# Kernel tuning notes

Hardware: AMD Instinct MI355X
Metric: run time of the kernel (lower is better)

## Reference

```python
import jax, jax.numpy as jnp
import numpy as np

D_MODEL = 2048
NUM_HEADS = 16
HEAD_DIM = D_MODEL // NUM_HEADS


def setup_inputs() -> dict:
    key = jax.random.key(0)
    ks = jax.random.split(key, 11)
    B, S = 2, 2048
    scale = 1.0 / np.sqrt(D_MODEL)
    inp = {
        "q": jax.random.normal(ks[0], (B, S, D_MODEL), jnp.float32),
        "k": jax.random.normal(ks[1], (B, S, D_MODEL), jnp.float32),
        "v": jax.random.normal(ks[2], (B, S, D_MODEL), jnp.float32),
        "Wq": jax.random.normal(ks[3], (D_MODEL, D_MODEL), jnp.float32) * scale,
        "bq": jnp.zeros((D_MODEL,), jnp.float32),
        "Wk": jax.random.normal(ks[4], (D_MODEL, D_MODEL), jnp.float32) * scale,
        "bk": jnp.zeros((D_MODEL,), jnp.float32),
        "Wv": jax.random.normal(ks[5], (D_MODEL, D_MODEL), jnp.float32) * scale,
        "bv": jnp.zeros((D_MODEL,), jnp.float32),
        "Wo": jax.random.normal(ks[6], (D_MODEL, D_MODEL), jnp.float32) * scale,
        "bo": jnp.zeros((D_MODEL,), jnp.float32),
    }
    return inp


def reference(q, k, v, Wq, bq, Wk, bk, Wv, bv, Wo, bo):
    B, S, _ = q.shape
    # projections (torch Linear: x @ W.T + b)
    qh = (q @ Wq.T + bq).reshape(B, S, NUM_HEADS, HEAD_DIM).transpose(0, 2, 1, 3)
    kh = (k @ Wk.T + bk).reshape(B, S, NUM_HEADS, HEAD_DIM).transpose(0, 2, 1, 3)
    vh = (v @ Wv.T + bv).reshape(B, S, NUM_HEADS, HEAD_DIM).transpose(0, 2, 1, 3)
    # scaled dot-product attention, full O(S^2) scores as in original
    scores = jnp.einsum("bhqd,bhkd->bhqk", qh, kh) / jnp.sqrt(
        jnp.asarray(HEAD_DIM, jnp.float32)
    )
    attn = jax.nn.softmax(scores, axis=-1)
    out = jnp.einsum("bhqk,bhkd->bhqd", attn, vh)
    out = out.transpose(0, 2, 1, 3).reshape(B, S, D_MODEL)
    return out @ Wo.T + bo
```

## Files before the change

### kernel.cpp

```cpp
#include <hip/hip_runtime.h>


typedef __attribute__((ext_vector_type(8))) short bf16x8;
typedef __attribute__((ext_vector_type(4))) float f32x4;
typedef __attribute__((ext_vector_type(8))) unsigned short u16x8;

__device__ __forceinline__ unsigned short f2bf(float f) {
  unsigned int u = __float_as_uint(f);
  u += 0x7fffu + ((u >> 16) & 1u);
  return (unsigned short)(u >> 16);
}

#if __has_builtin(__builtin_amdgcn_cvt_pk_bf16_f32)
__device__ __forceinline__ unsigned int pack2bf(float x, float y) {
  auto r = __builtin_amdgcn_cvt_pk_bf16_f32(x, y);
  return __builtin_bit_cast(unsigned int, r);
}
#else
__device__ __forceinline__ unsigned int pack2bf(float x, float y) {
  return (unsigned int)f2bf(x) | ((unsigned int)f2bf(y) << 16);
}
#endif

__device__ __forceinline__ float fast_exp2(float x) {
#if __has_builtin(__builtin_amdgcn_exp2f)
  return __builtin_amdgcn_exp2f(x);
#else
  return exp2f(x);
#endif
}

__device__ __forceinline__ void async16(const void* g, void* l) {
  __builtin_amdgcn_global_load_lds(
      (const __attribute__((address_space(1))) unsigned int*)g,
      (__attribute__((address_space(3))) unsigned int*)l, 16, 0, 0);
}

__device__ __forceinline__ f32x4 mfma_bf16(bf16x8 a, bf16x8 b, f32x4 c) {
  return __builtin_amdgcn_mfma_f32_16x16x32_bf16(a, b, c, 0, 0, 0);
}

__global__ __launch_bounds__(256) void cvt_kernel(
    const float* __restrict__ q, const float* __restrict__ k,
    const float* __restrict__ v, const float* __restrict__ Wq,
    const float* __restrict__ Wk, const float* __restrict__ Wv,
    const float* __restrict__ Wo, unsigned short* __restrict__ Xq,
    unsigned short* __restrict__ Xk, unsigned short* __restrict__ Xv,
    unsigned short* __restrict__ WqB, unsigned short* __restrict__ WkB,
    unsigned short* __restrict__ WvB, unsigned short* __restrict__ WoB) {
  size_t i = ((size_t)blockIdx.x * 256 + threadIdx.x) * 8;
  const float* src;
  unsigned short* dst;
  size_t off;
  if (i < 8388608ull) { src = q; dst = Xq; off = i; }
  else if (i < 16777216ull) { src = k; dst = Xk; off = i - 8388608ull; }
  else if (i < 25165824ull) { src = v; dst = Xv; off = i - 16777216ull; }
  else if (i < 29360128ull) { src = Wq; dst = WqB; off = i - 25165824ull; }
  else if (i < 33554432ull) { src = Wk; dst = WkB; off = i - 29360128ull; }
  else if (i < 37748736ull) { src = Wv; dst = WvB; off = i - 33554432ull; }
  else { src = Wo; dst = WoB; off = i - 37748736ull; }
  f32x4 a = *(const f32x4*)(src + off);
  f32x4 b = *(const f32x4*)(src + off + 4);
  u16x8 r;
  r[0] = f2bf(a[0]); r[1] = f2bf(a[1]); r[2] = f2bf(a[2]); r[3] = f2bf(a[3]);
  r[4] = f2bf(b[0]); r[5] = f2bf(b[1]); r[6] = f2bf(b[2]); r[7] = f2bf(b[3]);
  *(u16x8*)(dst + off) = r;
}

__device__ __forceinline__ void gemm_core_k2048(
    const unsigned short* __restrict__ A, const unsigned short* __restrict__ Bm,
    int m0, int n0, unsigned short* As, unsigned short* Bs,
    f32x4 (&acc)[4][4]) {
  const int tid = threadIdx.x;
  const int lane = tid & 63;
  const int wave = tid >> 6;
  const int quad = lane >> 4;
  const int l15 = lane & 15;
  const int wmt = (wave >> 1) * 4;
  const int wnt = (wave & 1) * 4;
  const int K = 2048;

  auto stage = [&](int kt, int buf) {
    unsigned short* SA = As + buf * (128 * 64);
    unsigned short* SB = Bs + buf * (128 * 64);
#pragma unroll
    for (int p = 0; p < 4; ++p) {
      int x = p * 256 + tid;
      int row = ((x >> 7) << 4) + ((x >> 3) & 15);
      int gk = kt + (((x & 7) ^ ((x >> 3) & 7)) << 3);
      async16(A + (size_t)(m0 + row) * K + gk,
              (char*)SA + (size_t)(p * 256 + wave * 64) * 16);
      async16(Bm + (size_t)(n0 + row) * K + gk,
              (char*)SB + (size_t)(p * 256 + wave * 64) * 16);
    }
  };
  stage(0, 0);
#pragma unroll 1
  for (int it = 0; it < 32; ++it) {
    __syncthreads();
    if (it + 1 < 32) stage((it + 1) * 64, (it + 1) & 1);
    const unsigned short* SA = As + (it & 1) * (128 * 64);
    const unsigned short* SB = Bs + (it & 1) * (128 * 64);
#pragma unroll
    for (int s = 0; s < 2; ++s) {
      const int cs = (s * 4 + quad) ^ (l15 & 7);
      bf16x8 af[4], bfr[4];
#pragma unroll
      for (int t = 0; t < 4; ++t) {
        af[t] = *(const bf16x8*)(SA + ((wmt + t) * 128 + l15 * 8 + cs) * 8);
        bfr[t] = *(const bf16x8*)(SB + ((wnt + t) * 128 + l15 * 8 + cs) * 8);
      }
#pragma unroll
      for (int mt = 0; mt < 4; ++mt)
#pragma unroll
        for (int nt = 0; nt < 4; ++nt)
          acc[mt][nt] = mfma_bf16(af[mt], bfr[nt], acc[mt][nt]);
    }
  }
}

__global__ __launch_bounds__(256, 2) void qkv_gemm(
    const unsigned short* __restrict__ Xq, const unsigned short* __restrict__ Xk,
    const unsigned short* __restrict__ Xv, const unsigned short* __restrict__ Wq,
    const unsigned short* __restrict__ Wk, const unsigned short* __restrict__ Wv,
    const float* __restrict__ bq, const float* __restrict__ bk,
    const float* __restrict__ bv, unsigned short* __restrict__ Qb,
    unsigned short* __restrict__ Kb, unsigned short* __restrict__ Vt) {
  __shared__ unsigned short As[2][128 * 64];
  __shared__ unsigned short Bs[2][128 * 64];
  const int z = blockIdx.z;
  const unsigned short* A = z == 0 ? Xq : z == 1 ? Xk : Xv;
  const unsigned short* Bm = z == 0 ? Wq : z == 1 ? Wk : Wv;
  const float* bias = z == 0 ? bq : z == 1 ? bk : bv;
  const int m0 = blockIdx.y * 128;
  const int n0 = blockIdx.x * 128;

  f32x4 acc[4][4];
#pragma unroll
  for (int i = 0; i < 4; ++i)
#pragma unroll
    for (int j = 0; j < 4; ++j) acc[i][j] = f32x4{0.f, 0.f, 0.f, 0.f};
  gemm_core_k2048(A, Bm, m0, n0, As[0], Bs[0], acc);

  const int lane = threadIdx.x & 63;
  const int wave = threadIdx.x >> 6;
  const int quad = lane >> 4;
  const int l15 = lane & 15;
  const int wmt = (wave >> 1) * 4;
  const int wnt = (wave & 1) * 4;
  const float SK = z == 0 ? 0.12753102331285527f : 1.0f;
  const int N = 2048;

#pragma unroll
  for (int nt = 0; nt < 4; ++nt) {
    int col = n0 + (wnt + nt) * 16 + l15;
    float bv_ = bias[col];
    if (z == 2) {
      int h = col >> 7, d = col & 127;
#pragma unroll
      for (int mt = 0; mt < 4; ++mt) {
        int row0 = m0 + (wmt + mt) * 16 + quad * 4;
        int bb = row0 >> 11, s = row0 & 2047;
        uint2 pk;
        pk.x = pack2bf(acc[mt][nt][0] + bv_, acc[mt][nt][1] + bv_);
        pk.y = pack2bf(acc[mt][nt][2] + bv_, acc[mt][nt][3] + bv_);
        *(uint2*)(Vt + ((size_t)((bb * 16 + h) * 128 + d)) * 2048 + s) = pk;
      }
    } else {
      unsigned short* C = z == 0 ? Qb : Kb;
#pragma unroll
      for (int mt = 0; mt < 4; ++mt) {
        int row0 = m0 + (wmt + mt) * 16 + quad * 4;
#pragma unroll
        for (int r = 0; r < 4; ++r)
          C[(size_t)(row0 + r) * N + col] = f2bf((acc[mt][nt][r] + bv_) * SK);
      }
    }
  }
}

__global__ __launch_bounds__(256, 2) void o_gemm(
    const unsigned short* __restrict__ A, const unsigned short* __restrict__ Bm,
    const float* __restrict__ bias, float* __restrict__ Cf) {
  __shared__ unsigned short As[2][128 * 64];
  __shared__ unsigned short Bs[2][128 * 64];
  const int m0 = blockIdx.y * 128;
  const int n0 = blockIdx.x * 128;

  f32x4 acc[4][4];
#pragma unroll
  for (int i = 0; i < 4; ++i)
#pragma unroll
    for (int j = 0; j < 4; ++j) acc[i][j] = f32x4{0.f, 0.f, 0.f, 0.f};
  gemm_core_k2048(A, Bm, m0, n0, As[0], Bs[0], acc);

  const int lane = threadIdx.x & 63;
  const int wave = threadIdx.x >> 6;
  const int quad = lane >> 4;
  const int l15 = lane & 15;
  const int wmt = (wave >> 1) * 4;
  const int wnt = (wave & 1) * 4;
  const int N = 2048;
#pragma unroll
  for (int nt = 0; nt < 4; ++nt) {
    int col = n0 + (wnt + nt) * 16 + l15;
    float bv_ = bias[col];
#pragma unroll
    for (int mt = 0; mt < 4; ++mt) {
      int row0 = m0 + (wmt + mt) * 16 + quad * 4;
#pragma unroll
      for (int r = 0; r < 4; ++r)
        Cf[(size_t)(row0 + r) * N + col] = acc[mt][nt][r] + bv_;
    }
  }
}

__global__ __launch_bounds__(256, 2) void attn_kernel(
    const unsigned short* __restrict__ Qg, const unsigned short* __restrict__ Kg,
    const unsigned short* __restrict__ Vt, unsigned short* __restrict__ ctx) {
  __shared__ unsigned short Ks[2][64 * 128];
  __shared__ unsigned short Vs[2][128 * 64];
  __shared__ unsigned short Ps[128 * 64];
  const int tid = threadIdx.x;
  const int lane = tid & 63;
  const int wave = tid >> 6;
  const int quad = lane >> 4;
  const int l15 = lane & 15;
  const int qt = blockIdx.x, h = blockIdx.y, b = blockIdx.z;
  const int q0 = qt * 128;
  const int swz = (l15 & 7) * 8;

  bf16x8 aq[2][4];
#pragma unroll
  for (int mt = 0; mt < 2; ++mt) {
    const unsigned short* qrow =
        Qg + (size_t)(b * 2048 + q0 + wave * 32 + mt * 16 + l15) * 2048 + h * 128;
#pragma unroll
    for (int ks = 0; ks < 4; ++ks)
      aq[mt][ks] = *(const bf16x8*)(qrow + ks * 32 + quad * 8);
  }

  f32x4 o[2][8];
#pragma unroll
  for (int mt = 0; mt < 2; ++mt)
#pragma unroll
    for (int dt = 0; dt < 8; ++dt) o[mt][dt] = f32x4{0.f, 0.f, 0.f, 0.f};
  f32x4 lacc[2] = {f32x4{0.f, 0.f, 0.f, 0.f}, f32x4{0.f, 0.f, 0.f, 0.f}};

  auto stage = [&](int t, int buf) {
#pragma unroll
    for (int p = 0; p < 4; ++p) {
      int slot = p * 256 + tid;
      {
        int nt = slot >> 8, c = (slot >> 4) & 15, r15 = slot & 15;
        const unsigned short* g =
            Kg + (size_t)(b * 2048 + t * 64 + nt * 16 + r15) * 2048 + h * 128 + c * 8;
        async16(g, (char*)Ks[buf] + (size_t)(p * 256 + wave * 64) * 16);
      }
      {
        int dt = slot >> 7, c = (slot >> 4) & 7, n15 = slot & 15;
        const unsigned short* g =
            Vt + ((size_t)(b * 16 + h) * 128 + dt * 16 + n15) * 2048 + t * 64 + c * 8;
        async16(g, (char*)Vs[buf] + (size_t)(p * 256 + wave * 64) * 16);
      }
    }
  };
  stage(0, 0);

  for (int t = 0; t < 32; ++t) {
    __syncthreads();
    if (t + 1 < 32) stage(t + 1, (t + 1) & 1);
    const unsigned short* Kb = Ks[t & 1];
    const unsigned short* Vb = Vs[t & 1];

    f32x4 sc[2][4];
#pragma unroll
    for (int nt = 0; nt < 4; ++nt) {
      sc[0][nt] = f32x4{0.f, 0.f, 0.f, 0.f};
      sc[1][nt] = f32x4{0.f, 0.f, 0.f, 0.f};
#pragma unroll
      for (int ks = 0; ks < 4; ++ks) {
        bf16x8 bk = *(const bf16x8*)(Kb + (nt * 256 + (ks * 4 + quad) * 16 + l15) * 8);
        sc[0][nt] = mfma_bf16(bk, aq[0][ks], sc[0][nt]);
        sc[1][nt] = mfma_bf16(bk, aq[1][ks], sc[1][nt]);
      }
    }

#pragma unroll
    for (int mt = 0; mt < 2; ++mt) {
      int prow = (wave * 32 + mt * 16 + l15) * 64;
#pragma unroll
      for (int nt = 0; nt < 4; ++nt) {
        f32x4 p;
#pragma unroll
        for (int r = 0; r < 4; ++r) p[r] = fast_exp2(sc[mt][nt][r]);
        lacc[mt] += p;
        uint2 pk;
        pk.x = pack2bf(p[0], p[1]);
        pk.y = pack2bf(p[2], p[3]);
        *(uint2*)(Ps + prow + ((nt * 16 + quad * 4) ^ swz)) = pk;
      }
    }

    bf16x8 ap[2][2];
#pragma unroll
    for (int mt = 0; mt < 2; ++mt) {
      int prow = (wave * 32 + mt * 16 + l15) * 64;
#pragma unroll
      for (int ks = 0; ks < 2; ++ks)
        ap[mt][ks] = *(const bf16x8*)(Ps + prow + ((ks * 32 + quad * 8) ^ swz));
    }
#pragma unroll
    for (int dt = 0; dt < 8; ++dt) {
#pragma unroll
      for (int ks = 0; ks < 2; ++ks) {
        bf16x8 bv = *(const bf16x8*)(Vb + (dt * 128 + (ks * 4 + quad) * 16 + l15) * 8);
        o[0][dt] = mfma_bf16(ap[0][ks], bv, o[0][dt]);
        o[1][dt] = mfma_bf16(ap[1][ks], bv, o[1][dt]);
      }
    }
  }

  float lq[2];
#pragma unroll
  for (int mt = 0; mt < 2; ++mt) {
    float s = lacc[mt][0] + lacc[mt][1] + lacc[mt][2] + lacc[mt][3];
    s += __shfl_xor(s, 16, 64);
    s += __shfl_xor(s, 32, 64);
    lq[mt] = s;
  }

#pragma unroll
  for (int mt = 0; mt < 2; ++mt) {
#pragma unroll
    for (int r = 0; r < 4; ++r) {
      float lr = __shfl(lq[mt], quad * 4 + r, 64);
      float inv = 1.0f / lr;
      unsigned short* crow =
          ctx + (size_t)(b * 2048 + q0 + wave * 32 + mt * 16 + quad * 4 + r) * 2048 +
          h * 128;
#pragma unroll
      for (int dt = 0; dt < 8; ++dt)
        crow[dt * 16 + l15] = f2bf(o[mt][dt][r] * inv);
    }
  }
}

extern "C" void kernel_launch(void* const* d_in, const int* in_sizes, int n_in,
                              void* d_out, int out_size, void* d_ws,
                              size_t ws_size, hipStream_t stream) {
  const float* q = (const float*)d_in[0];
  const float* k = (const float*)d_in[1];
  const float* v = (const float*)d_in[2];
  const float* Wq = (const float*)d_in[3];
  const float* bq = (const float*)d_in[4];
  const float* Wk = (const float*)d_in[5];
  const float* bk = (const float*)d_in[6];
  const float* Wv = (const float*)d_in[7];
  const float* bv = (const float*)d_in[8];
  const float* Wo = (const float*)d_in[9];
  const float* bo = (const float*)d_in[10];
  float* out = (float*)d_out;

  char* ws = (char*)d_ws;
  const size_t MB = 1024 * 1024;
  unsigned short* Xq  = (unsigned short*)(ws + 0 * MB);
  unsigned short* Xk  = (unsigned short*)(ws + 16 * MB);
  unsigned short* Xv  = (unsigned short*)(ws + 32 * MB);
  unsigned short* WqB = (unsigned short*)(ws + 48 * MB);
  unsigned short* WkB = (unsigned short*)(ws + 56 * MB);
  unsigned short* WvB = (unsigned short*)(ws + 64 * MB);
  unsigned short* WoB = (unsigned short*)(ws + 72 * MB);
  unsigned short* Qb  = (unsigned short*)(ws + 80 * MB);
  unsigned short* Kb  = (unsigned short*)(ws + 96 * MB);
  unsigned short* Vt  = (unsigned short*)(ws + 112 * MB);
  unsigned short* ctx = Xq;

  cvt_kernel<<<20480, 256, 0, stream>>>(q, k, v, Wq, Wk, Wv, Wo, Xq, Xk, Xv,
                                        WqB, WkB, WvB, WoB);
  qkv_gemm<<<dim3(16, 32, 3), 256, 0, stream>>>(Xq, Xk, Xv, WqB, WkB, WvB, bq,
                                                bk, bv, Qb, Kb, Vt);
  attn_kernel<<<dim3(16, 16, 2), 256, 0, stream>>>(Qb, Kb, Vt, ctx);
  o_gemm<<<dim3(16, 32), 256, 0, stream>>>(ctx, WoB, bo, out);
}
```

Measured before the change: 456.2 us.

## Switch GEMM core to triple-buffered BK=32 pipeline with partial vmcnt waits

The shared GEMM core used by the QKV and output projections now stages 32-wide K tiles into three LDS buffers instead of two 64-wide buffers. It waits with an explicit s_waitcnt vmcnt(4) plus barrier so one prefetch stays in flight while computing, and it shrinks LDS per block so occupancy can rise to 3 blocks per CU. The hardware packed bf16 conversion is also dropped in favour of the software rounding path. The risk is more barriers per K step, a smaller compute chunk per sync, and slower bias/pack epilogues.

```diff
diff --git a/kernel.cpp b/kernel.cpp
--- a/kernel.cpp
+++ b/kernel.cpp
@@ -11,16 +11,9 @@
   return (unsigned short)(u >> 16);
 }
 
-#if __has_builtin(__builtin_amdgcn_cvt_pk_bf16_f32)
-__device__ __forceinline__ unsigned int pack2bf(float x, float y) {
-  auto r = __builtin_amdgcn_cvt_pk_bf16_f32(x, y);
-  return __builtin_bit_cast(unsigned int, r);
-}
-#else
 __device__ __forceinline__ unsigned int pack2bf(float x, float y) {
   return (unsigned int)f2bf(x) | ((unsigned int)f2bf(y) << 16);
 }
-#endif
 
 __device__ __forceinline__ float fast_exp2(float x) {
 #if __has_builtin(__builtin_amdgcn_exp2f)
@@ -38,6 +31,13 @@
 
 __device__ __forceinline__ f32x4 mfma_bf16(bf16x8 a, bf16x8 b, f32x4 c) {
   return __builtin_amdgcn_mfma_f32_16x16x32_bf16(a, b, c, 0, 0, 0);
+}
+
+__device__ __forceinline__ void wait4_barrier() {
+  asm volatile("s_waitcnt vmcnt(4)\n\ts_barrier" ::: "memory");
+}
+__device__ __forceinline__ void wait0_barrier() {
+  asm volatile("s_waitcnt vmcnt(0)\n\ts_barrier" ::: "memory");
 }
 
 __global__ __launch_bounds__(256) void cvt_kernel(
@@ -81,53 +81,63 @@
   const int K = 2048;
 
   auto stage = [&](int kt, int buf) {
-    unsigned short* SA = As + buf * (128 * 64);
-    unsigned short* SB = Bs + buf * (128 * 64);
-#pragma unroll
-    for (int p = 0; p < 4; ++p) {
+    unsigned short* SA = As + buf * (128 * 32);
+    unsigned short* SB = Bs + buf * (128 * 32);
+#pragma unroll
+    for (int p = 0; p < 2; ++p) {
       int x = p * 256 + tid;
-      int row = ((x >> 7) << 4) + ((x >> 3) & 15);
-      int gk = kt + (((x & 7) ^ ((x >> 3) & 7)) << 3);
+      int row = ((x >> 6) << 4) + ((x >> 2) & 15);
+      int gk = kt + (((x & 3) ^ ((x >> 2) & 3)) << 3);
       async16(A + (size_t)(m0 + row) * K + gk,
               (char*)SA + (size_t)(p * 256 + wave * 64) * 16);
       async16(Bm + (size_t)(n0 + row) * K + gk,
               (char*)SB + (size_t)(p * 256 + wave * 64) * 16);
     }
   };
+  auto compute = [&](int buf) {
+    const unsigned short* SA = As + buf * (128 * 32);
+    const unsigned short* SB = Bs + buf * (128 * 32);
+    const int cs = quad ^ (l15 & 3);
+    bf16x8 af[4], bfr[4];
+#pragma unroll
+    for (int t = 0; t < 4; ++t) {
+      af[t] = *(const bf16x8*)(SA + ((wmt + t) * 64 + l15 * 4 + cs) * 8);
+      bfr[t] = *(const bf16x8*)(SB + ((wnt + t) * 64 + l15 * 4 + cs) * 8);
+    }
+#pragma unroll
+    for (int mt = 0; mt < 4; ++mt)
+#pragma unroll
+      for (int nt = 0; nt < 4; ++nt)
+        acc[mt][nt] = mfma_bf16(af[mt], bfr[nt], acc[mt][nt]);
+  };
+
   stage(0, 0);
+  stage(32, 1);
+  int cbuf = 0, sbuf = 2;
 #pragma unroll 1
-  for (int it = 0; it < 32; ++it) {
-    __syncthreads();
-    if (it + 1 < 32) stage((it + 1) * 64, (it + 1) & 1);
-    const unsigned short* SA = As + (it & 1) * (128 * 64);
-    const unsigned short* SB = Bs + (it & 1) * (128 * 64);
-#pragma unroll
-    for (int s = 0; s < 2; ++s) {
-      const int cs = (s * 4 + quad) ^ (l15 & 7);
-      bf16x8 af[4], bfr[4];
-#pragma unroll
-      for (int t = 0; t < 4; ++t) {
-        af[t] = *(const bf16x8*)(SA + ((wmt + t) * 128 + l15 * 8 + cs) * 8);
-        bfr[t] = *(const bf16x8*)(SB + ((wnt + t) * 128 + l15 * 8 + cs) * 8);
-      }
-#pragma unroll
-      for (int mt = 0; mt < 4; ++mt)
-#pragma unroll
-        for (int nt = 0; nt < 4; ++nt)
-          acc[mt][nt] = mfma_bf16(af[mt], bfr[nt], acc[mt][nt]);
-    }
-  }
-}
-
-__global__ __launch_bounds__(256, 2) void qkv_gemm(
+  for (int it = 0; it < 62; ++it) {
+    wait4_barrier();
+    stage((it + 2) * 32, sbuf);
+    compute(cbuf);
+    cbuf = cbuf == 2 ? 0 : cbuf + 1;
+    sbuf = sbuf == 2 ? 0 : sbuf + 1;
+  }
+  wait4_barrier();
+  compute(cbuf);
+  cbuf = cbuf == 2 ? 0 : cbuf + 1;
+  wait0_barrier();
+  compute(cbuf);
+}
+
+__global__ __launch_bounds__(256, 3) void qkv_gemm(
     const unsigned short* __restrict__ Xq, const unsigned short* __restrict__ Xk,
     const unsigned short* __restrict__ Xv, const unsigned short* __restrict__ Wq,
     const unsigned short* __restrict__ Wk, const unsigned short* __restrict__ Wv,
     const float* __restrict__ bq, const float* __restrict__ bk,
     const float* __restrict__ bv, unsigned short* __restrict__ Qb,
     unsigned short* __restrict__ Kb, unsigned short* __restrict__ Vt) {
-  __shared__ unsigned short As[2][128 * 64];
-  __shared__ unsigned short Bs[2][128 * 64];
+  __shared__ unsigned short As[3][128 * 32];
+  __shared__ unsigned short Bs[3][128 * 32];
   const int z = blockIdx.z;
   const unsigned short* A = z == 0 ? Xq : z == 1 ? Xk : Xv;
   const unsigned short* Bm = z == 0 ? Wq : z == 1 ? Wk : Wv;
@@ -179,11 +189,11 @@
   }
 }
 
-__global__ __launch_bounds__(256, 2) void o_gemm(
+__global__ __launch_bounds__(256, 3) void o_gemm(
     const unsigned short* __restrict__ A, const unsigned short* __restrict__ Bm,
     const float* __restrict__ bias, float* __restrict__ Cf) {
-  __shared__ unsigned short As[2][128 * 64];
-  __shared__ unsigned short Bs[2][128 * 64];
+  __shared__ unsigned short As[3][128 * 32];
+  __shared__ unsigned short Bs[3][128 * 32];
   const int m0 = blockIdx.y * 128;
   const int n0 = blockIdx.x * 128;
 
```

Measured after the change: 479.2 us. +5.0%, slower.

## Widen QKV GEMM tile to 128x256 with BK=32 staging

Applied to the files above, without the earlier changes.

Replaces the QKV projection's 128x128 tile (BK=64) with a 128x256 tile and BK=32 double buffering, so each wave computes a 4x8 MFMA block and B fragments are streamed per column tile. The aim is more MFMA work per A fragment load and fewer LDS/global loads per flop, with launch bounds raised to 3 blocks per CU. The trade-off is more accumulator registers, twice as many K iterations with their barriers, and half as many blocks. The builtin packed bf16 conversion is also replaced with the manual rounding path.

```diff
diff --git a/kernel.cpp b/kernel.cpp
--- a/kernel.cpp
+++ b/kernel.cpp
@@ -11,16 +11,9 @@
   return (unsigned short)(u >> 16);
 }
 
-#if __has_builtin(__builtin_amdgcn_cvt_pk_bf16_f32)
-__device__ __forceinline__ unsigned int pack2bf(float x, float y) {
-  auto r = __builtin_amdgcn_cvt_pk_bf16_f32(x, y);
-  return __builtin_bit_cast(unsigned int, r);
-}
-#else
 __device__ __forceinline__ unsigned int pack2bf(float x, float y) {
   return (unsigned int)f2bf(x) | ((unsigned int)f2bf(y) << 16);
 }
-#endif
 
 __device__ __forceinline__ float fast_exp2(float x) {
 #if __has_builtin(__builtin_amdgcn_exp2f)
@@ -67,7 +60,68 @@
   *(u16x8*)(dst + off) = r;
 }
 
-__device__ __forceinline__ void gemm_core_k2048(
+__device__ __forceinline__ void gemm_core_wide(
+    const unsigned short* __restrict__ A, const unsigned short* __restrict__ Bm,
+    int m0, int n0, unsigned short* As, unsigned short* Bs,
+    f32x4 (&acc)[4][8]) {
+  const int tid = threadIdx.x;
+  const int lane = tid & 63;
+  const int wave = tid >> 6;
+  const int quad = lane >> 4;
+  const int l15 = lane & 15;
+  const int wm = (wave >> 1) * 4;
+  const int wn = (wave & 1) * 8;
+  const int K = 2048;
+
+  auto stage = [&](int kt, int buf) {
+    unsigned short* SA = As + buf * (128 * 32);
+    unsigned short* SB = Bs + buf * (256 * 32);
+#pragma unroll
+    for (int p = 0; p < 2; ++p) {
+      int x = p * 256 + tid;
+      int r15 = (x >> 3) & 15, pair = x >> 7, u = x & 7;
+      int w = u ^ (r15 & 7);
+      int row = (pair * 2 + (w >> 2)) * 16 + r15;
+      int gk = kt + (w & 3) * 8;
+      async16(A + (size_t)(m0 + row) * K + gk, (char*)SA + (size_t)x * 16);
+    }
+#pragma unroll
+    for (int p = 0; p < 4; ++p) {
+      int x = p * 256 + tid;
+      int r15 = (x >> 3) & 15, pair = x >> 7, u = x & 7;
+      int w = u ^ (r15 & 7);
+      int row = (pair * 2 + (w >> 2)) * 16 + r15;
+      int gk = kt + (w & 3) * 8;
+      async16(Bm + (size_t)(n0 + row) * K + gk, (char*)SB + (size_t)x * 16);
+    }
+  };
+
+  auto rd_frag = [&](const unsigned short* S, int t16) -> bf16x8 {
+    int v = (((t16 & 1) << 2) | quad) ^ (l15 & 7);
+    return *(const bf16x8*)(S + (((t16 >> 1) * 128 + l15 * 8 + v) << 3));
+  };
+
+  stage(0, 0);
+#pragma unroll 1
+  for (int it = 0; it < 64; ++it) {
+    __syncthreads();
+    if (it + 1 < 64) stage((it + 1) * 32, (it + 1) & 1);
+    const unsigned short* SA = As + (it & 1) * (128 * 32);
+    const unsigned short* SB = Bs + (it & 1) * (256 * 32);
+    bf16x8 af[4];
+#pragma unroll
+    for (int t = 0; t < 4; ++t) af[t] = rd_frag(SA, wm + t);
+#pragma unroll
+    for (int nt = 0; nt < 8; ++nt) {
+      bf16x8 bfr = rd_frag(SB, wn + nt);
+#pragma unroll
+      for (int mt = 0; mt < 4; ++mt)
+        acc[mt][nt] = mfma_bf16(af[mt], bfr, acc[mt][nt]);
+    }
+  }
+}
+
+__device__ __forceinline__ void gemm_core_bk64(
     const unsigned short* __restrict__ A, const unsigned short* __restrict__ Bm,
     int m0, int n0, unsigned short* As, unsigned short* Bs,
     f32x4 (&acc)[4][4]) {
@@ -119,47 +173,47 @@
   }
 }
 
-__global__ __launch_bounds__(256, 2) void qkv_gemm(
+__global__ __launch_bounds__(256, 3) void qkv_gemm(
     const unsigned short* __restrict__ Xq, const unsigned short* __restrict__ Xk,
     const unsigned short* __restrict__ Xv, const unsigned short* __restrict__ Wq,
     const unsigned short* __restrict__ Wk, const unsigned short* __restrict__ Wv,
     const float* __restrict__ bq, const float* __restrict__ bk,
     const float* __restrict__ bv, unsigned short* __restrict__ Qb,
     unsigned short* __restrict__ Kb, unsigned short* __restrict__ Vt) {
-  __shared__ unsigned short As[2][128 * 64];
-  __shared__ unsigned short Bs[2][128 * 64];
+  __shared__ unsigned short As[2][128 * 32];
+  __shared__ unsigned short Bs[2][256 * 32];
   const int z = blockIdx.z;
   const unsigned short* A = z == 0 ? Xq : z == 1 ? Xk : Xv;
   const unsigned short* Bm = z == 0 ? Wq : z == 1 ? Wk : Wv;
   const float* bias = z == 0 ? bq : z == 1 ? bk : bv;
   const int m0 = blockIdx.y * 128;
-  const int n0 = blockIdx.x * 128;
-
-  f32x4 acc[4][4];
+  const int n0 = blockIdx.x * 256;
+
+  f32x4 acc[4][8];
 #pragma unroll
   for (int i = 0; i < 4; ++i)
 #pragma unroll
-    for (int j = 0; j < 4; ++j) acc[i][j] = f32x4{0.f, 0.f, 0.f, 0.f};
-  gemm_core_k2048(A, Bm, m0, n0, As[0], Bs[0], acc);
+    for (int j = 0; j < 8; ++j) acc[i][j] = f32x4{0.f, 0.f, 0.f, 0.f};
+  gemm_core_wide(A, Bm, m0, n0, As[0], Bs[0], acc);
 
   const int lane = threadIdx.x & 63;
   const int wave = threadIdx.x >> 6;
   const int quad = lane >> 4;
   const int l15 = lane & 15;
-  const int wmt = (wave >> 1) * 4;
-  const int wnt = (wave & 1) * 4;
+  const int wm = (wave >> 1) * 4;
+  const int wn = (wave & 1) * 8;
   const float SK = z == 0 ? 0.12753102331285527f : 1.0f;
   const int N = 2048;
 
 #pragma unroll
-  for (int nt = 0; nt < 4; ++nt) {
-    int col = n0 + (wnt + nt) * 16 + l15;
+  for (int nt = 0; nt < 8; ++nt) {
+    int col = n0 + (wn + nt) * 16 + l15;
     float bv_ = bias[col];
     if (z == 2) {
       int h = col >> 7, d = col & 127;
 #pragma unroll
       for (int mt = 0; mt < 4; ++mt) {
-        int row0 = m0 + (wmt + mt) * 16 + quad * 4;
+        int row0 = m0 + (wm + mt) * 16 + quad * 4;
         int bb = row0 >> 11, s = row0 & 2047;
         uint2 pk;
         pk.x = pack2bf(acc[mt][nt][0] + bv_, acc[mt][nt][1] + bv_);
@@ -170,7 +224,7 @@
       unsigned short* C = z == 0 ? Qb : Kb;
 #pragma unroll
       for (int mt = 0; mt < 4; ++mt) {
-        int row0 = m0 + (wmt + mt) * 16 + quad * 4;
+        int row0 = m0 + (wm + mt) * 16 + quad * 4;
 #pragma unroll
         for (int r = 0; r < 4; ++r)
           C[(size_t)(row0 + r) * N + col] = f2bf((acc[mt][nt][r] + bv_) * SK);
@@ -192,7 +246,7 @@
   for (int i = 0; i < 4; ++i)
 #pragma unroll
     for (int j = 0; j < 4; ++j) acc[i][j] = f32x4{0.f, 0.f, 0.f, 0.f};
-  gemm_core_k2048(A, Bm, m0, n0, As[0], Bs[0], acc);
+  gemm_core_bk64(A, Bm, m0, n0, As[0], Bs[0], acc);
 
   const int lane = threadIdx.x & 63;
   const int wave = threadIdx.x >> 6;
@@ -378,8 +432,8 @@
 
   cvt_kernel<<<20480, 256, 0, stream>>>(q, k, v, Wq, Wk, Wv, Wo, Xq, Xk, Xv,
                                         WqB, WkB, WvB, WoB);
-  qkv_gemm<<<dim3(16, 32, 3), 256, 0, stream>>>(Xq, Xk, Xv, WqB, WkB, WvB, bq,
-                                                bk, bv, Qb, Kb, Vt);
+  qkv_gemm<<<dim3(8, 32, 3), 256, 0, stream>>>(Xq, Xk, Xv, WqB, WkB, WvB, bq,
+                                               bk, bv, Qb, Kb, Vt);
   attn_kernel<<<dim3(16, 16, 2), 256, 0, stream>>>(Qb, Kb, Vt, ctx);
   o_gemm<<<dim3(16, 32), 256, 0, stream>>>(ctx, WoB, bo, out);
 }
```

Measured after the change: 491.1 us. 7.7% more time.
